# Optimization experiments

Hardware: AMD Instinct MI355X
Metric: run time of the kernel (lower is better)

The kernel has to match this reference:

```python
import jax, jax.numpy as jnp
import numpy as np

B, A, V, D = 16, 1024, 1024, 512


def setup_inputs() -> dict:
    key = jax.random.key(0)
    k1, k2 = jax.random.split(key)
    audio_encoded = jax.random.normal(k1, (B, A, D), dtype=jnp.float32)
    visual_encoded = jax.random.normal(k2, (B, V, D), dtype=jnp.float32)
    return {"audio_encoded": audio_encoded, "visual_encoded": visual_encoded}


def reference(audio_encoded, visual_encoded):
    # Batched pairwise L2 distance: out[b, a, v] = ||audio[b,a] - visual[b,v]||_2
    # Fused ||a||^2 + ||v||^2 - 2 a.v formulation (single batched GEMM) replacing
    # the original per-(batch, audio-frame) Python loop of diff/pow/sum/sqrt.
    a_sq = jnp.sum(audio_encoded * audio_encoded, axis=-1)   # [B, A]
    v_sq = jnp.sum(visual_encoded * visual_encoded, axis=-1)  # [B, V]
    cross = jnp.einsum("bad,bvd->bav", audio_encoded, visual_encoded)  # [B, A, V]
    dist_sq = a_sq[:, :, None] + v_sq[:, None, :] - 2.0 * cross
    dist_sq = jnp.maximum(dist_sq, 0.0)  # clamp fp round-off negatives
    l2_features = jnp.sqrt(dist_sq)  # [B, A, V]
    return l2_features
```

## Files before the change

kernel.cpp:

```cpp
#include <hip/hip_runtime.h>
#include <hip/hip_bf16.h>

typedef __attribute__((ext_vector_type(8))) short short8;
typedef __attribute__((ext_vector_type(4))) float fv4;

constexpr int B_ = 16, A_ = 1024, V_ = 1024, D_ = 512;

__device__ __forceinline__ unsigned cvtpk(float lo, float hi) {
    unsigned r;
    asm("v_cvt_pk_bf16_f32 %0, %1, %2" : "=v"(r) : "v"(lo), "v"(hi));
    return r;
}
__device__ __forceinline__ unsigned lds_addr(const void* p) {
    return (unsigned)(unsigned long long)(__attribute__((address_space(3))) const char*)p;
}
__device__ __forceinline__ short8 dsr128(unsigned a) {
    short8 r;
    asm volatile("ds_read_b128 %0, %1" : "=v"(r) : "v"(a));
    return r;
}
#define SB0()  __builtin_amdgcn_sched_barrier(0)
#define LGK0() asm volatile("s_waitcnt lgkmcnt(0)")
#define BARX() do { SB0(); LGK0(); __builtin_amdgcn_s_barrier(); SB0(); } while (0)

struct Stage { fv4 x0, x1, x2, x3; };

__global__ void __launch_bounds__(256, 2)
l2dist_fused128(const float* __restrict__ audio, const float* __restrict__ visual,
                float* __restrict__ out)
{
    __shared__ __align__(16) char sA[2][128 * 128];
    __shared__ __align__(16) char sB[2][128 * 128];
    __shared__ float lnrm[256];

    const int t = threadIdx.x, lane = t & 63, w = t >> 6;
    const int wm = w >> 1, wn = w & 1;

    const int orig = blockIdx.x;
    const int wg   = (orig & 7) * 128 + (orig >> 3);
    const int b = wg >> 6, tile = wg & 63, ab = tile >> 3, vb = tile & 7;

    const float* Ag = audio  + ((size_t)b * A_ + ab * 128) * D_;
    const float* Vg = visual + ((size_t)b * V_ + vb * 128) * D_;

    const int rg  = t >> 2;
    const int lq  = t & 3;
    const int key = rg & 7;

    const float* g0 = Ag + (size_t)rg * D_ + lq * 4;
    const float* g1 = Ag + (size_t)(64 + rg) * D_ + lq * 4;
    const float* g2 = Vg + (size_t)rg * D_ + lq * 4;
    const float* g3 = Vg + (size_t)(64 + rg) * D_ + lq * 4;

    const int oLo = rg * 128;
    const int oHi = (64 + rg) * 128;

    float ps0 = 0.f, ps1 = 0.f, ps2 = 0.f, ps3 = 0.f;

#define ISSUE(S, gbase, koff) do {                                   \
        const float* _p = (gbase) + (koff);                          \
        S.x0 = *(const fv4*)(_p);      S.x1 = *(const fv4*)(_p + 16);\
        S.x2 = *(const fv4*)(_p + 32); S.x3 = *(const fv4*)(_p + 48);\
    } while (0)

#define PROC(S, dst, rowoff, ps) do {                                            \
        ps += S.x0[0]*S.x0[0] + S.x0[1]*S.x0[1] + S.x0[2]*S.x0[2] + S.x0[3]*S.x0[3] \
            + S.x1[0]*S.x1[0] + S.x1[1]*S.x1[1] + S.x1[2]*S.x1[2] + S.x1[3]*S.x1[3] \
            + S.x2[0]*S.x2[0] + S.x2[1]*S.x2[1] + S.x2[2]*S.x2[2] + S.x2[3]*S.x2[3] \
            + S.x3[0]*S.x3[0] + S.x3[1]*S.x3[1] + S.x3[2]*S.x3[2] + S.x3[3]*S.x3[3];\
        char* _d = (dst) + (rowoff);                                             \
        { int2 _v; _v.x = (int)cvtpk(S.x0[0], S.x0[1]); _v.y = (int)cvtpk(S.x0[2], S.x0[3]); \
          *(int2*)(_d + ((((0 + (lq >> 1)) ^ key) << 4) + (lq & 1) * 8)) = _v; } \
        { int2 _v; _v.x = (int)cvtpk(S.x1[0], S.x1[1]); _v.y = (int)cvtpk(S.x1[2], S.x1[3]); \
          *(int2*)(_d + ((((2 + (lq >> 1)) ^ key) << 4) + (lq & 1) * 8)) = _v; } \
        { int2 _v; _v.x = (int)cvtpk(S.x2[0], S.x2[1]); _v.y = (int)cvtpk(S.x2[2], S.x2[3]); \
          *(int2*)(_d + ((((4 + (lq >> 1)) ^ key) << 4) + (lq & 1) * 8)) = _v; } \
        { int2 _v; _v.x = (int)cvtpk(S.x3[0], S.x3[1]); _v.y = (int)cvtpk(S.x3[2], S.x3[3]); \
          *(int2*)(_d + ((((6 + (lq >> 1)) ^ key) << 4) + (lq & 1) * 8)) = _v; } \
    } while (0)

    {
        Stage p0, p1, p2, p3;
        ISSUE(p0, g0, 0); ISSUE(p1, g1, 0); ISSUE(p2, g2, 0); ISSUE(p3, g3, 0); SB0();
        PROC(p0, (char*)sA[0], oLo, ps0);
        PROC(p1, (char*)sA[0], oHi, ps1);
        PROC(p2, (char*)sB[0], oLo, ps2);
        PROC(p3, (char*)sB[0], oHi, ps3);
    }
    __syncthreads();

    fv4 acc[4][4];
#pragma unroll
    for (int m = 0; m < 4; ++m)
#pragma unroll
        for (int n = 0; n < 4; ++n) acc[m][n] = fv4{0.f, 0.f, 0.f, 0.f};

    const int frow = lane & 15, fg = lane >> 4, xk = frow & 7;
    const unsigned cof0 = (unsigned)(((0 + fg) ^ xk) << 4);
    const unsigned cof1 = (unsigned)(((4 + fg) ^ xk) << 4);
    const unsigned baseA = lds_addr(&sA[0][0]);
    const unsigned baseB = lds_addr(&sB[0][0]);
    const unsigned arow = (unsigned)((wm * 64 + frow) * 128);
    const unsigned brow = (unsigned)((wn * 64 + frow) * 128);

#pragma unroll 1
    for (int kt = 0; kt < 8; ++kt) {
        const int cur = kt & 1;
        char* dA = (char*)sA[cur ^ 1];
        char* dB = (char*)sB[cur ^ 1];
        const unsigned Ab = baseA + (unsigned)cur * 16384u + arow;
        const unsigned Bb = baseB + (unsigned)cur * 16384u + brow;
        const int koff = (kt + 1) * 64;
        const bool st = (kt < 7);

        Stage q0, q1, q2, q3;
        if (st) { ISSUE(q0, g0, koff); ISSUE(q1, g1, koff);
                  ISSUE(q2, g2, koff); ISSUE(q3, g3, koff); SB0(); }

        short8 av[4][2];
        {
            short8 bv[2][2];
#pragma unroll
            for (int m = 0; m < 4; ++m) {
                av[m][0] = dsr128(Ab + m * 2048 + cof0);
                av[m][1] = dsr128(Ab + m * 2048 + cof1);
            }
#pragma unroll
            for (int n = 0; n < 2; ++n) {
                bv[n][0] = dsr128(Bb + n * 2048 + cof0);
                bv[n][1] = dsr128(Bb + n * 2048 + cof1);
            }
            LGK0(); SB0();
            __builtin_amdgcn_s_setprio(1);
#pragma unroll
            for (int k = 0; k < 2; ++k)
#pragma unroll
                for (int m = 0; m < 4; ++m)
#pragma unroll
                    for (int n = 0; n < 2; ++n)
                        acc[m][n] = __builtin_amdgcn_mfma_f32_16x16x32_bf16(av[m][k], bv[n][k], acc[m][n], 0, 0, 0);
            __builtin_amdgcn_s_setprio(0);
        }
        if (st) { PROC(q0, dA, oLo, ps0); PROC(q1, dA, oHi, ps1); }

        {
            short8 bv[2][2];
#pragma unroll
            for (int n = 0; n < 2; ++n) {
                bv[n][0] = dsr128(Bb + (n + 2) * 2048 + cof0);
                bv[n][1] = dsr128(Bb + (n + 2) * 2048 + cof1);
            }
            LGK0(); SB0();
            __builtin_amdgcn_s_setprio(1);
#pragma unroll
            for (int k = 0; k < 2; ++k)
#pragma unroll
                for (int m = 0; m < 4; ++m)
#pragma unroll
                    for (int n = 0; n < 2; ++n)
                        acc[m][n + 2] = __builtin_amdgcn_mfma_f32_16x16x32_bf16(av[m][k], bv[n][k], acc[m][n + 2], 0, 0, 0);
            __builtin_amdgcn_s_setprio(0);
        }
        if (st) { PROC(q2, dB, oLo, ps2); PROC(q3, dB, oHi, ps3); }

        BARX();
    }

    ps0 += __shfl_xor(ps0, 1, 64); ps0 += __shfl_xor(ps0, 2, 64);
    ps1 += __shfl_xor(ps1, 1, 64); ps1 += __shfl_xor(ps1, 2, 64);
    ps2 += __shfl_xor(ps2, 1, 64); ps2 += __shfl_xor(ps2, 2, 64);
    ps3 += __shfl_xor(ps3, 1, 64); ps3 += __shfl_xor(ps3, 2, 64);
    if (lq == 0) {
        lnrm[rg]       = ps0;
        lnrm[64 + rg]  = ps1;
        lnrm[128 + rg] = ps2;
        lnrm[192 + rg] = ps3;
    }
    __syncthreads();

    float* Ob = out + (size_t)b * A_ * V_ + (size_t)(ab * 128) * V_ + vb * 128;
#pragma unroll
    for (int m = 0; m < 4; ++m) {
#pragma unroll
        for (int n = 0; n < 4; ++n) {
            const int col = wn * 64 + n * 16 + frow;
            const float vsq = lnrm[128 + col];
#pragma unroll
            for (int j = 0; j < 4; ++j) {
                const int row = wm * 64 + m * 16 + fg * 4 + j;
                float d2 = lnrm[row] + vsq - 2.f * acc[m][n][j];
                Ob[(size_t)row * V_ + col] = sqrtf(fmaxf(d2, 0.f));
            }
        }
    }
#undef ISSUE
#undef PROC
}

extern "C" void kernel_launch(void* const* d_in, const int* in_sizes, int n_in,
                              void* d_out, int out_size, void* d_ws, size_t ws_size,
                              hipStream_t stream) {
    const float* audio  = (const float*)d_in[0];
    const float* visual = (const float*)d_in[1];
    float* out = (float*)d_out;
    l2dist_fused128<<<1024, 256, 0, stream>>>(audio, visual, out);
}
```

Before: 48.45 us.

## Split into bf16 convert/norm prepass and direct-to-LDS bf16 GEMM kernel

After: 49.54 us. +2.2%, slower.

```diff
diff --git a/kernel.cpp b/kernel.cpp
--- a/kernel.cpp
+++ b/kernel.cpp
@@ -3,13 +3,58 @@
 
 typedef __attribute__((ext_vector_type(8))) short short8;
 typedef __attribute__((ext_vector_type(4))) float fv4;
+typedef __attribute__((ext_vector_type(4))) int   iv4;
 
 constexpr int B_ = 16, A_ = 1024, V_ = 1024, D_ = 512;
-
-__device__ __forceinline__ unsigned cvtpk(float lo, float hi) {
-    unsigned r;
-    asm("v_cvt_pk_bf16_f32 %0, %1, %2" : "=v"(r) : "v"(lo), "v"(hi));
-    return r;
+constexpr int ROWS_A = B_ * A_;
+constexpr int ROWS_T = 2 * ROWS_A;
+constexpr size_t BF_ONE = (size_t)ROWS_A * D_ * 2;
+constexpr size_t WS_NEED = 2 * BF_ONE + (size_t)ROWS_T * 4;
+
+__device__ __forceinline__ unsigned f2bf(float f) {
+    unsigned u = __builtin_bit_cast(unsigned, f);
+    return (u + 0x7fffu + ((u >> 16) & 1u)) >> 16;
+}
+
+__global__ void __launch_bounds__(256)
+convert_kernel(const float* __restrict__ audio, const float* __restrict__ visual,
+               ushort* __restrict__ abf, ushort* __restrict__ vbf,
+               float* __restrict__ normA, float* __restrict__ normV)
+{
+    const int lane = threadIdx.x & 63;
+    const int wv   = (blockIdx.x * 256 + threadIdx.x) >> 6;
+    const int nw   = (gridDim.x * 256) >> 6;
+
+    for (int row = wv; row < ROWS_T; row += nw) {
+        const float* src; ushort* dst; float* nd; int r;
+        if (row < ROWS_A) { src = audio;  dst = abf; nd = normA; r = row; }
+        else              { src = visual; dst = vbf; nd = normV; r = row - ROWS_A; }
+
+        const float* p = src + (size_t)r * D_ + lane * 8;
+        fv4 x0 = *(const fv4*)p;
+        fv4 x1 = *(const fv4*)(p + 4);
+
+        float s = 0.f;
+#pragma unroll
+        for (int i = 0; i < 4; ++i) s += x0[i] * x0[i] + x1[i] * x1[i];
+
+        iv4 w;
+        w[0] = (int)(f2bf(x0[0]) | (f2bf(x0[1]) << 16));
+        w[1] = (int)(f2bf(x0[2]) | (f2bf(x0[3]) << 16));
+        w[2] = (int)(f2bf(x1[0]) | (f2bf(x1[1]) << 16));
+        w[3] = (int)(f2bf(x1[2]) | (f2bf(x1[3]) << 16));
+        *(iv4*)(dst + (size_t)r * D_ + lane * 8) = w;
+
+#pragma unroll
+        for (int m = 1; m < 64; m <<= 1) s += __shfl_xor(s, m, 64);
+        if (lane == 0) nd[r] = s;
+    }
+}
+
+__device__ __forceinline__ void gload16(const void* g, void* l) {
+    __builtin_amdgcn_global_load_lds((const __attribute__((address_space(1))) void*)g,
+                                     (__attribute__((address_space(3))) void*)l,
+                                     16, 0, 0);
 }
 __device__ __forceinline__ unsigned lds_addr(const void* p) {
     return (unsigned)(unsigned long long)(__attribute__((address_space(3))) const char*)p;
@@ -19,15 +64,15 @@
     asm volatile("ds_read_b128 %0, %1" : "=v"(r) : "v"(a));
     return r;
 }
-#define SB0()  __builtin_amdgcn_sched_barrier(0)
-#define LGK0() asm volatile("s_waitcnt lgkmcnt(0)")
-#define BARX() do { SB0(); LGK0(); __builtin_amdgcn_s_barrier(); SB0(); } while (0)
-
-struct Stage { fv4 x0, x1, x2, x3; };
+#define SB0()   __builtin_amdgcn_sched_barrier(0)
+#define LGK0()  asm volatile("s_waitcnt lgkmcnt(0)")
+#define VMCN(n) asm volatile("s_waitcnt vmcnt(" #n ")")
+#define RBAR()  do { SB0(); __builtin_amdgcn_s_barrier(); SB0(); } while (0)
 
 __global__ void __launch_bounds__(256, 2)
-l2dist_fused128(const float* __restrict__ audio, const float* __restrict__ visual,
-                float* __restrict__ out)
+gemm128(const ushort* __restrict__ abf, const ushort* __restrict__ vbf,
+        const float* __restrict__ normA, const float* __restrict__ normV,
+        float* __restrict__ out)
 {
     __shared__ __align__(16) char sA[2][128 * 128];
     __shared__ __align__(16) char sB[2][128 * 128];
@@ -40,54 +85,36 @@
     const int wg   = (orig & 7) * 128 + (orig >> 3);
     const int b = wg >> 6, tile = wg & 63, ab = tile >> 3, vb = tile & 7;
 
-    const float* Ag = audio  + ((size_t)b * A_ + ab * 128) * D_;
-    const float* Vg = visual + ((size_t)b * V_ + vb * 128) * D_;
-
-    const int rg  = t >> 2;
-    const int lq  = t & 3;
-    const int key = rg & 7;
-
-    const float* g0 = Ag + (size_t)rg * D_ + lq * 4;
-    const float* g1 = Ag + (size_t)(64 + rg) * D_ + lq * 4;
-    const float* g2 = Vg + (size_t)rg * D_ + lq * 4;
-    const float* g3 = Vg + (size_t)(64 + rg) * D_ + lq * 4;
-
-    const int oLo = rg * 128;
-    const int oHi = (64 + rg) * 128;
-
-    float ps0 = 0.f, ps1 = 0.f, ps2 = 0.f, ps3 = 0.f;
-
-#define ISSUE(S, gbase, koff) do {                                   \
-        const float* _p = (gbase) + (koff);                          \
-        S.x0 = *(const fv4*)(_p);      S.x1 = *(const fv4*)(_p + 16);\
-        S.x2 = *(const fv4*)(_p + 32); S.x3 = *(const fv4*)(_p + 48);\
+    const ushort* Ag = abf + ((size_t)b * A_ + ab * 128) * D_;
+    const ushort* Vg = vbf + ((size_t)b * V_ + vb * 128) * D_;
+
+    const int rl = lane >> 3;
+    const int cs = (lane & 7) ^ rl;
+    const ushort* asrc = Ag + (size_t)(w * 32 + rl) * D_ + cs * 8;
+    const ushort* vsrc = Vg + (size_t)(w * 32 + rl) * D_ + cs * 8;
+
+#define STAGE(kt, buf) do {                                           \
+        const size_t _ko = (size_t)(kt) * 64;                         \
+        char* _da = (char*)sA[buf] + w * 32 * 128;                    \
+        char* _db = (char*)sB[buf] + w * 32 * 128;                    \
+        gload16(asrc + 0 * 8 * D_ + _ko, _da + 0 * 1024);             \
+        gload16(vsrc + 0 * 8 * D_ + _ko, _db + 0 * 1024);             \
+        gload16(asrc + 1 * 8 * D_ + _ko, _da + 1 * 1024);             \
+        gload16(vsrc + 1 * 8 * D_ + _ko, _db + 1 * 1024);             \
+        gload16(asrc + 2 * 8 * D_ + _ko, _da + 2 * 1024);             \
+        gload16(vsrc + 2 * 8 * D_ + _ko, _db + 2 * 1024);             \
+        gload16(asrc + 3 * 8 * D_ + _ko, _da + 3 * 1024);             \
+        gload16(vsrc + 3 * 8 * D_ + _ko, _db + 3 * 1024);             \
     } while (0)
 
-#define PROC(S, dst, rowoff, ps) do {                                            \
-        ps += S.x0[0]*S.x0[0] + S.x0[1]*S.x0[1] + S.x0[2]*S.x0[2] + S.x0[3]*S.x0[3] \
-            + S.x1[0]*S.x1[0] + S.x1[1]*S.x1[1] + S.x1[2]*S.x1[2] + S.x1[3]*S.x1[3] \
-            + S.x2[0]*S.x2[0] + S.x2[1]*S.x2[1] + S.x2[2]*S.x2[2] + S.x2[3]*S.x2[3] \
-            + S.x3[0]*S.x3[0] + S.x3[1]*S.x3[1] + S.x3[2]*S.x3[2] + S.x3[3]*S.x3[3];\
-        char* _d = (dst) + (rowoff);                                             \
-        { int2 _v; _v.x = (int)cvtpk(S.x0[0], S.x0[1]); _v.y = (int)cvtpk(S.x0[2], S.x0[3]); \
-          *(int2*)(_d + ((((0 + (lq >> 1)) ^ key) << 4) + (lq & 1) * 8)) = _v; } \
-        { int2 _v; _v.x = (int)cvtpk(S.x1[0], S.x1[1]); _v.y = (int)cvtpk(S.x1[2], S.x1[3]); \
-          *(int2*)(_d + ((((2 + (lq >> 1)) ^ key) << 4) + (lq & 1) * 8)) = _v; } \
-        { int2 _v; _v.x = (int)cvtpk(S.x2[0], S.x2[1]); _v.y = (int)cvtpk(S.x2[2], S.x2[3]); \
-          *(int2*)(_d + ((((4 + (lq >> 1)) ^ key) << 4) + (lq & 1) * 8)) = _v; } \
-        { int2 _v; _v.x = (int)cvtpk(S.x3[0], S.x3[1]); _v.y = (int)cvtpk(S.x3[2], S.x3[3]); \
-          *(int2*)(_d + ((((6 + (lq >> 1)) ^ key) << 4) + (lq & 1) * 8)) = _v; } \
-    } while (0)
-
-    {
-        Stage p0, p1, p2, p3;
-        ISSUE(p0, g0, 0); ISSUE(p1, g1, 0); ISSUE(p2, g2, 0); ISSUE(p3, g3, 0); SB0();
-        PROC(p0, (char*)sA[0], oLo, ps0);
-        PROC(p1, (char*)sA[0], oHi, ps1);
-        PROC(p2, (char*)sB[0], oLo, ps2);
-        PROC(p3, (char*)sB[0], oHi, ps3);
-    }
+    if (t < 128) lnrm[t] = normA[(size_t)b * A_ + ab * 128 + t];
+    else         lnrm[t] = normV[(size_t)b * V_ + vb * 128 + (t - 128)];
     __syncthreads();
+
+    STAGE(0, 0);
+    STAGE(1, 1);
+    VMCN(8);
+    RBAR();
 
     fv4 acc[4][4];
 #pragma unroll
@@ -106,16 +133,8 @@
 #pragma unroll 1
     for (int kt = 0; kt < 8; ++kt) {
         const int cur = kt & 1;
-        char* dA = (char*)sA[cur ^ 1];
-        char* dB = (char*)sB[cur ^ 1];
         const unsigned Ab = baseA + (unsigned)cur * 16384u + arow;
         const unsigned Bb = baseB + (unsigned)cur * 16384u + brow;
-        const int koff = (kt + 1) * 64;
-        const bool st = (kt < 7);
-
-        Stage q0, q1, q2, q3;
-        if (st) { ISSUE(q0, g0, koff); ISSUE(q1, g1, koff);
-                  ISSUE(q2, g2, koff); ISSUE(q3, g3, koff); SB0(); }
 
         short8 av[4][2];
         {
@@ -141,8 +160,6 @@
                         acc[m][n] = __builtin_amdgcn_mfma_f32_16x16x32_bf16(av[m][k], bv[n][k], acc[m][n], 0, 0, 0);
             __builtin_amdgcn_s_setprio(0);
         }
-        if (st) { PROC(q0, dA, oLo, ps0); PROC(q1, dA, oHi, ps1); }
-
         {
             short8 bv[2][2];
 #pragma unroll
@@ -161,22 +178,18 @@
                         acc[m][n + 2] = __builtin_amdgcn_mfma_f32_16x16x32_bf16(av[m][k], bv[n][k], acc[m][n + 2], 0, 0, 0);
             __builtin_amdgcn_s_setprio(0);
         }
-        if (st) { PROC(q2, dB, oLo, ps2); PROC(q3, dB, oHi, ps3); }
-
-        BARX();
-    }
-
-    ps0 += __shfl_xor(ps0, 1, 64); ps0 += __shfl_xor(ps0, 2, 64);
-    ps1 += __shfl_xor(ps1, 1, 64); ps1 += __shfl_xor(ps1, 2, 64);
-    ps2 += __shfl_xor(ps2, 1, 64); ps2 += __shfl_xor(ps2, 2, 64);
-    ps3 += __shfl_xor(ps3, 1, 64); ps3 += __shfl_xor(ps3, 2, 64);
-    if (lq == 0) {
-        lnrm[rg]       = ps0;
-        lnrm[64 + rg]  = ps1;
-        lnrm[128 + rg] = ps2;
-        lnrm[192 + rg] = ps3;
-    }
-    __syncthreads();
+
+        if (kt < 7) {
+            RBAR();
+            if (kt < 6) {
+                STAGE(kt + 2, cur);
+                VMCN(8);
+            } else {
+                VMCN(0);
+            }
+            RBAR();
+        }
+    }
 
     float* Ob = out + (size_t)b * A_ * V_ + (size_t)(ab * 128) * V_ + vb * 128;
 #pragma unroll
@@ -193,8 +206,27 @@
             }
         }
     }
-#undef ISSUE
-#undef PROC
+#undef STAGE
+}
+
+__global__ void __launch_bounds__(256)
+l2dist_naive(const float* __restrict__ audio, const float* __restrict__ visual,
+             float* __restrict__ out)
+{
+    const size_t idx = (size_t)blockIdx.x * 256 + threadIdx.x;
+    const size_t total = (size_t)B_ * A_ * V_;
+    if (idx >= total) return;
+    const int v = idx & (V_ - 1);
+    const int a = (idx >> 10) & (A_ - 1);
+    const int b = idx >> 20;
+    const float* ap = audio  + ((size_t)b * A_ + a) * D_;
+    const float* vp = visual + ((size_t)b * V_ + v) * D_;
+    float s = 0.f;
+    for (int d = 0; d < D_; ++d) {
+        float df = ap[d] - vp[d];
+        s += df * df;
+    }
+    out[idx] = sqrtf(s);
 }
 
 extern "C" void kernel_launch(void* const* d_in, const int* in_sizes, int n_in,
@@ -203,5 +235,17 @@
     const float* audio  = (const float*)d_in[0];
     const float* visual = (const float*)d_in[1];
     float* out = (float*)d_out;
-    l2dist_fused128<<<1024, 256, 0, stream>>>(audio, visual, out);
-}
+
+    if (ws_size >= WS_NEED) {
+        char* ws = (char*)d_ws;
+        ushort* abf = (ushort*)ws;
+        ushort* vbf = (ushort*)(ws + BF_ONE);
+        float*  nA  = (float*)(ws + 2 * BF_ONE);
+        float*  nV  = nA + ROWS_A;
+        convert_kernel<<<2048, 256, 0, stream>>>(audio, visual, abf, vbf, nA, nV);
+        gemm128<<<1024, 256, 0, stream>>>(abf, vbf, nA, nV, out);
+    } else {
+        const size_t total = (size_t)B_ * A_ * V_;
+        l2dist_naive<<<(int)((total + 255) / 256), 256, 0, stream>>>(audio, visual, out);
+    }
+}
```
